# Kernel optimization log

Measured on AMD Instinct MI355X. Metric: run time of the kernel, lower is better.

Reference implementation:

```python
import jax, jax.numpy as jnp
import numpy as np


def _cofactor_antieq(M):
    """ith output = M[...,i,0] * (-1)**i * det(M with row i and col 0 deleted).

    M: (..., n, n) -> (..., n). Vectorized form of the original per-row
    jnp.delete + stack + det construction.
    """
    n = M.shape[-1]
    # rows[i] = all row indices except i, shape (n, n-1)
    rows = np.stack([np.delete(np.arange(n), i) for i in range(n)])
    Msub = M[..., 1:]                 # delete first column: (..., n, n-1)
    sub = Msub[..., rows, :]          # delete row i per output: (..., n, n-1, n-1)
    signs = jnp.asarray((-1.0) ** np.arange(n), dtype=M.dtype)
    return M[..., 0] * signs * jnp.linalg.det(sub)


def setup_inputs() -> dict:
    key = jax.random.key(0)
    ks = jax.random.split(key, 6)
    B, NSPIN, NPS, D, NION, DIM = 4096, 2, 16, 256, 8, 3
    eq_inputs = jax.random.normal(ks[0], (B, NSPIN * NPS, D), jnp.float32)
    r_ei = jax.random.normal(ks[1], (B, NSPIN * NPS, NION, DIM), jnp.float32)
    # per-spin linear orbital params (stacked over spin since splits are equal)
    W = jax.random.normal(ks[2], (NSPIN, D, NPS), jnp.float32) / np.sqrt(D)
    b = jax.random.normal(ks[3], (NSPIN, NPS), jnp.float32) * 0.01
    # anisotropic envelope decay matrices A per (spin, ion, orbital), near identity
    env_dim = jax.random.normal(ks[4], (NSPIN, NION, NPS, DIM, DIM), jnp.float32) * 0.1 + jnp.eye(DIM, dtype=jnp.float32)
    # linear combination over ions per (spin, orbital)
    env_ion = jax.random.normal(ks[5], (NSPIN, NION, NPS), jnp.float32) / NION
    return dict(eq_inputs=eq_inputs, r_ei=r_ei, W=W, b=b, env_dim=env_dim, env_ion=env_ion)


def reference(eq_inputs, r_ei, W, b, env_dim, env_ion):
    B = eq_inputs.shape[0]
    nspin, d, nps = W.shape
    nion, dim = r_ei.shape[-2], r_ei.shape[-1]
    # split particles by spin: (B, nspin, nps, ...)
    xs = eq_inputs.reshape(B, nspin, nps, d)
    rs = r_ei.reshape(B, nspin, nps, nion, dim)
    # linear part of orbitals: (B, s, n, o) with n = o = nps (square per spin)
    y = jnp.einsum('bsnd,sdo->bsno', xs, W) + b[:, None, :]
    # anisotropic exponential envelope: exp(-||A (r - R)||), summed over ions
    Ar = jnp.einsum('sioed,bsnid->bsnioe', env_dim, rs)        # (B,s,n,ion,orb,3)
    env = jnp.einsum('bsnio,sio->bsno',
                     jnp.exp(-jnp.linalg.norm(Ar, axis=-1)), env_ion)
    M = y * env                                                 # (B, s, n, n)
    cof = _cofactor_antieq(M)                                   # (B, s, n)
    return cof[..., None]                                       # (B, s, n, 1)
```

## Files before the change

### kernel.cpp

```cpp
#include <hip/hip_runtime.h>
#include <math.h>


__global__ __launch_bounds__(256)
void cof_fused(const float* __restrict__ eq,
               const float* __restrict__ rei,
               const float* __restrict__ Wm,
               const float* __restrict__ bb,
               const float* __restrict__ edim,
               const float* __restrict__ eion,
               float* __restrict__ out)
{
  __shared__ __align__(16) float Gl[8 * 6 * 16];
  __shared__ __align__(16) float Xl[4 * 2048];

  const int tid   = threadIdx.x;
  const int lane  = tid & 63;
  const int wv    = tid >> 6;
  const int blk   = blockIdx.x;
  const int sp    = blk >> 10;
  const int bbase = (blk & 1023) * 4;

  if (tid < 128) {
    const int i = tid >> 4, o = tid & 15;
    const float* A = edim + (((size_t)sp * 8 + i) * 16 + o) * 9;
    const float a0=A[0],a1=A[1],a2=A[2],a3=A[3],a4=A[4],a5=A[5],a6=A[6],a7=A[7],a8=A[8];
    float* Gp = Gl + i * 96 + o;
    Gp[0]  = a0*a0 + a3*a3 + a6*a6;
    Gp[16] = a1*a1 + a4*a4 + a7*a7;
    Gp[32] = a2*a2 + a5*a5 + a8*a8;
    Gp[48] = 2.f*(a0*a1 + a3*a4 + a6*a7);
    Gp[64] = 2.f*(a0*a2 + a3*a5 + a6*a8);
    Gp[80] = 2.f*(a1*a2 + a4*a5 + a7*a8);
  }
  __syncthreads();

  const int bidx = bbase + wv;
  const int cch  = lane >> 4;
  const int nb   = (lane >> 2) & 3;
  const int ob   = lane & 3;

  const float* xb = eq + ((size_t)bidx * 32 + sp * 16) * 256;
  const float* wb = Wm + (size_t)sp * 4096;
  float* xw = Xl + wv * 2048;

  const int srow = 2 * 0 + (lane >> 5);
  const int schk = lane & 31;

  float acc[4][4] = {{0.f,0.f,0.f,0.f},{0.f,0.f,0.f,0.f},
                     {0.f,0.f,0.f,0.f},{0.f,0.f,0.f,0.f}};

  float4 st[8];
  #pragma unroll
  for (int t = 0; t < 8; ++t)
    st[t] = *(const float4*)(xb + (2 * t + (lane >> 5)) * 256 + schk * 4);
  #pragma unroll
  for (int t = 0; t < 8; ++t) {
    const int row = 2 * t + (lane >> 5);
    *(float4*)(xw + row * 128 + (schk ^ (row & 7)) * 4) = st[t];
  }
  float4 st2[8];
  #pragma unroll
  for (int t = 0; t < 8; ++t)
    st2[t] = *(const float4*)(xb + (2 * t + (lane >> 5)) * 256 + 128 + schk * 4);

  #pragma unroll 2
  for (int q = 0; q < 8; ++q) {
    const int d0 = q * 16 + cch * 4;
    float xr[4][4], wr[4][4];
    #pragma unroll
    for (int r = 0; r < 4; ++r) {
      const int n = 4 * nb + r;
      float4 t = *(const float4*)(xw + n * 128 + ((q * 4 + cch) ^ (n & 7)) * 4);
      xr[r][0]=t.x; xr[r][1]=t.y; xr[r][2]=t.z; xr[r][3]=t.w;
    }
    #pragma unroll
    for (int j = 0; j < 4; ++j) {
      float4 t = *(const float4*)(wb + (d0 + j) * 16 + 4 * ob);
      wr[j][0]=t.x; wr[j][1]=t.y; wr[j][2]=t.z; wr[j][3]=t.w;
    }
    #pragma unroll
    for (int r = 0; r < 4; ++r)
      #pragma unroll
      for (int j = 0; j < 4; ++j)
        #pragma unroll
        for (int c2 = 0; c2 < 4; ++c2)
          acc[r][c2] = fmaf(xr[r][j], wr[j][c2], acc[r][c2]);
  }

  #pragma unroll
  for (int t = 0; t < 8; ++t) {
    const int row = 2 * t + (lane >> 5);
    *(float4*)(xw + row * 128 + (schk ^ (row & 7)) * 4) = st2[t];
  }
  #pragma unroll 2
  for (int q = 0; q < 8; ++q) {
    const int d0 = 128 + q * 16 + cch * 4;
    float xr[4][4], wr[4][4];
    #pragma unroll
    for (int r = 0; r < 4; ++r) {
      const int n = 4 * nb + r;
      float4 t = *(const float4*)(xw + n * 128 + ((q * 4 + cch) ^ (n & 7)) * 4);
      xr[r][0]=t.x; xr[r][1]=t.y; xr[r][2]=t.z; xr[r][3]=t.w;
    }
    #pragma unroll
    for (int j = 0; j < 4; ++j) {
      float4 t = *(const float4*)(wb + (d0 + j) * 16 + 4 * ob);
      wr[j][0]=t.x; wr[j][1]=t.y; wr[j][2]=t.z; wr[j][3]=t.w;
    }
    #pragma unroll
    for (int r = 0; r < 4; ++r)
      #pragma unroll
      for (int j = 0; j < 4; ++j)
        #pragma unroll
        for (int c2 = 0; c2 < 4; ++c2)
          acc[r][c2] = fmaf(xr[r][j], wr[j][c2], acc[r][c2]);
  }

  #pragma unroll
  for (int r = 0; r < 4; ++r)
    #pragma unroll
    for (int c2 = 0; c2 < 4; ++c2) {
      float v = acc[r][c2];
      v += __shfl_xor(v, 16);
      v += __shfl_xor(v, 32);
      acc[r][c2] = v;
    }

  float* Mw = xw;
  {
    float4 bv = *(const float4*)(bb + sp * 16 + 4 * ob);
    if (lane < 16) {
      #pragma unroll
      for (int r = 0; r < 4; ++r) {
        float4 v = make_float4(acc[r][0] + bv.x, acc[r][1] + bv.y,
                               acc[r][2] + bv.z, acc[r][3] + bv.w);
        *(float4*)(Mw + (4 * nb + r) * 20 + 4 * ob) = v;
      }
    }
  }

  {
    const int n = lane >> 2;
    const float* rp = rei + ((size_t)bidx * 32 + sp * 16 + n) * 24;
    float rv[24];
    #pragma unroll
    for (int t4 = 0; t4 < 6; ++t4) {
      float4 t = *(const float4*)(rp + t4 * 4);
      rv[t4*4+0]=t.x; rv[t4*4+1]=t.y; rv[t4*4+2]=t.z; rv[t4*4+3]=t.w;
    }
    float4 env = make_float4(0.f, 0.f, 0.f, 0.f);
    #pragma unroll
    for (int i = 0; i < 8; ++i) {
      const float r0 = rv[i*3], r1 = rv[i*3+1], r2 = rv[i*3+2];
      const float rr0 = r0*r0, rr1 = r1*r1, rr2 = r2*r2;
      const float rr3 = r0*r1, rr4 = r0*r2, rr5 = r1*r2;
      const float* Gp = Gl + i * 96 + 4 * ob;
      const float4 q00 = *(const float4*)(Gp);
      const float4 q11 = *(const float4*)(Gp + 16);
      const float4 q22 = *(const float4*)(Gp + 32);
      const float4 q01 = *(const float4*)(Gp + 48);
      const float4 q02 = *(const float4*)(Gp + 64);
      const float4 q12 = *(const float4*)(Gp + 80);
      const float4 io  = *(const float4*)(eion + ((size_t)sp * 8 + i) * 16 + 4 * ob);
#define ENVC(c) { float n2 = q00.c*rr0 + q11.c*rr1 + q22.c*rr2 \
                           + q01.c*rr3 + q02.c*rr4 + q12.c*rr5; \
                  n2 = fmaxf(n2, 0.f); \
                  env.c += __expf(-sqrtf(n2)) * io.c; }
      ENVC(x) ENVC(y) ENVC(z) ENVC(w)
#undef ENVC
    }
    float* mp = Mw + n * 20 + 4 * ob;
    float4 y = *(const float4*)mp;
    *(float4*)mp = make_float4(y.x * env.x, y.y * env.y, y.z * env.z, y.w * env.w);
  }
  __syncthreads();

  if (wv == 0) {
    const int g  = lane >> 4;
    const int r  = lane & 15;
    const int gb = lane & 48;
    const float* mg = Xl + g * 2048;
    float a[16];
    #pragma unroll
    for (int c = 0; c < 16; ++c) a[c] = mg[c * 20 + r];

    float det = 1.0f;
    int sign = 0;
    unsigned retired = 0;
    int piv[16];
    int srr = 0;
    float accf = (r == 0) ? 1.0f : 0.0f;
    float acc2 = 0.0f;

    #pragma unroll
    for (int k = 0; k < 16; ++k) {
      const bool act = ((retired >> r) & 1u) == 0u;
      const float av = act ? fabsf(a[k]) : 0.0f;
      unsigned pk = (__float_as_uint(av) & 0xFFFFFFF0u) | (unsigned)r;
      #pragma unroll
      for (int m = 1; m <= 8; m <<= 1) {
        unsigned o2 = __shfl_xor(pk, m);
        pk = (pk > o2) ? pk : o2;
      }
      const int p = (int)(pk & 15u);
      piv[k] = p;
      float pv = __shfl(a[k], gb | p);
      if (fabsf(pv) < 1e-30f) pv = (pv < 0.0f) ? -1e-30f : 1e-30f;
      det *= pv;
      retired |= (1u << p);
      sign ^= (int)(__popc((~retired) & ((1u << p) - 1u)) & 1u);
      if (r == p) srr = k;
      const bool upd = act && (r != p);
      float m2 = 0.0f;
      if (upd) { m2 = a[k] / pv; a[k] = m2; }
      #pragma unroll
      for (int c = k + 1; c < 16; ++c) {
        float bcv = __shfl(a[c], gb | p);
        if (upd) a[c] = fmaf(-m2, bcv, a[c]);
      }
      float zk = __shfl(accf, gb | p);
      if (r == p) acc2 = zk;
      if (upd) accf = fmaf(-m2, zk, accf);
    }
    if (sign) det = -det;

    float myx = 0.0f;
    #pragma unroll
    for (int j = 15; j >= 0; --j) {
      float t = acc2 / a[j];
      float xj = __shfl(t, gb | piv[j]);
      if (srr < j) acc2 = fmaf(-a[j], xj, acc2);
      if (r == j) myx = xj;
    }

    const float mi0 = mg[r * 20];
    const float cof = mi0 * det * myx;
    out[((size_t)(bbase + g) * 2 + sp) * 16 + r] = cof;
  }
}

extern "C" void kernel_launch(void* const* d_in, const int* in_sizes, int n_in,
                              void* d_out, int out_size, void* d_ws, size_t ws_size,
                              hipStream_t stream) {
  (void)in_sizes; (void)n_in; (void)out_size; (void)d_ws; (void)ws_size;
  const float* eq   = (const float*)d_in[0];
  const float* rei  = (const float*)d_in[1];
  const float* Wm   = (const float*)d_in[2];
  const float* bb   = (const float*)d_in[3];
  const float* edim = (const float*)d_in[4];
  const float* eion = (const float*)d_in[5];
  float* out = (float*)d_out;
  hipLaunchKernelGGL(cof_fused, dim3(2048), dim3(256), 0, stream,
                     eq, rei, Wm, bb, edim, eion, out);
}
```

Before: 231.1 us.

## Shrink LDS staging, pipeline quarter loads, and run determinant per wave

Cuts the per-wave LDS staging buffer in half by streaming the 256-wide input in four 64-column quarters with double-buffered register loads overlapping compute. Drops the block barrier and the wave-0-only determinant phase, so each wave now computes the determinant of its own matrix, with only lanes 0-15 storing results. Packs pivot indices into two registers instead of an array and requests 7 waves per EU via launch bounds. These aim at higher occupancy and less serialization, at the cost of each wave doing redundant 4x-replicated determinant work across lane groups and added register pressure from the occupancy hint.

New measurement: 300.4 us. +30.0%, slower.

```diff
diff --git a/kernel.cpp b/kernel.cpp
--- a/kernel.cpp
+++ b/kernel.cpp
@@ -2,7 +2,7 @@
 #include <math.h>
 
 
-__global__ __launch_bounds__(256)
+__global__ __launch_bounds__(256, 7)
 void cof_fused(const float* __restrict__ eq,
                const float* __restrict__ rei,
                const float* __restrict__ Wm,
@@ -12,7 +12,7 @@
                float* __restrict__ out)
 {
   __shared__ __align__(16) float Gl[8 * 6 * 16];
-  __shared__ __align__(16) float Xl[4 * 2048];
+  __shared__ __align__(16) float Xl[4 * 1024];
 
   const int tid   = threadIdx.x;
   const int lane  = tid & 63;
@@ -42,80 +42,70 @@
 
   const float* xb = eq + ((size_t)bidx * 32 + sp * 16) * 256;
   const float* wb = Wm + (size_t)sp * 4096;
-  float* xw = Xl + wv * 2048;
-
-  const int srow = 2 * 0 + (lane >> 5);
-  const int schk = lane & 31;
+  float* xw = Xl + wv * 1024;
+
+  const int srow = lane >> 4;
+  const int schk = lane & 15;
 
   float acc[4][4] = {{0.f,0.f,0.f,0.f},{0.f,0.f,0.f,0.f},
                      {0.f,0.f,0.f,0.f},{0.f,0.f,0.f,0.f}};
 
-  float4 st[8];
-  #pragma unroll
-  for (int t = 0; t < 8; ++t)
-    st[t] = *(const float4*)(xb + (2 * t + (lane >> 5)) * 256 + schk * 4);
-  #pragma unroll
-  for (int t = 0; t < 8; ++t) {
-    const int row = 2 * t + (lane >> 5);
-    *(float4*)(xw + row * 128 + (schk ^ (row & 7)) * 4) = st[t];
-  }
-  float4 st2[8];
-  #pragma unroll
-  for (int t = 0; t < 8; ++t)
-    st2[t] = *(const float4*)(xb + (2 * t + (lane >> 5)) * 256 + 128 + schk * 4);
-
-  #pragma unroll 2
-  for (int q = 0; q < 8; ++q) {
-    const int d0 = q * 16 + cch * 4;
-    float xr[4][4], wr[4][4];
-    #pragma unroll
-    for (int r = 0; r < 4; ++r) {
-      const int n = 4 * nb + r;
-      float4 t = *(const float4*)(xw + n * 128 + ((q * 4 + cch) ^ (n & 7)) * 4);
-      xr[r][0]=t.x; xr[r][1]=t.y; xr[r][2]=t.z; xr[r][3]=t.w;
-    }
-    #pragma unroll
-    for (int j = 0; j < 4; ++j) {
-      float4 t = *(const float4*)(wb + (d0 + j) * 16 + 4 * ob);
-      wr[j][0]=t.x; wr[j][1]=t.y; wr[j][2]=t.z; wr[j][3]=t.w;
-    }
-    #pragma unroll
-    for (int r = 0; r < 4; ++r)
-      #pragma unroll
-      for (int j = 0; j < 4; ++j)
-        #pragma unroll
-        for (int c2 = 0; c2 < 4; ++c2)
-          acc[r][c2] = fmaf(xr[r][j], wr[j][c2], acc[r][c2]);
-  }
-
-  #pragma unroll
-  for (int t = 0; t < 8; ++t) {
-    const int row = 2 * t + (lane >> 5);
-    *(float4*)(xw + row * 128 + (schk ^ (row & 7)) * 4) = st2[t];
-  }
-  #pragma unroll 2
-  for (int q = 0; q < 8; ++q) {
-    const int d0 = 128 + q * 16 + cch * 4;
-    float xr[4][4], wr[4][4];
-    #pragma unroll
-    for (int r = 0; r < 4; ++r) {
-      const int n = 4 * nb + r;
-      float4 t = *(const float4*)(xw + n * 128 + ((q * 4 + cch) ^ (n & 7)) * 4);
-      xr[r][0]=t.x; xr[r][1]=t.y; xr[r][2]=t.z; xr[r][3]=t.w;
-    }
-    #pragma unroll
-    for (int j = 0; j < 4; ++j) {
-      float4 t = *(const float4*)(wb + (d0 + j) * 16 + 4 * ob);
-      wr[j][0]=t.x; wr[j][1]=t.y; wr[j][2]=t.z; wr[j][3]=t.w;
-    }
-    #pragma unroll
-    for (int r = 0; r < 4; ++r)
-      #pragma unroll
-      for (int j = 0; j < 4; ++j)
-        #pragma unroll
-        for (int c2 = 0; c2 < 4; ++c2)
-          acc[r][c2] = fmaf(xr[r][j], wr[j][c2], acc[r][c2]);
-  }
+  float4 stA[4], stB[4];
+
+#define LOADQ(dst, qq)                                                        \
+  _Pragma("unroll")                                                           \
+  for (int t = 0; t < 4; ++t)                                                 \
+    dst[t] = *(const float4*)(xb + (4 * t + srow) * 256 + (qq) * 64 + schk * 4);
+
+#define WRITEQ(src)                                                           \
+  _Pragma("unroll")                                                           \
+  for (int t = 0; t < 4; ++t) {                                               \
+    const int row_ = 4 * t + srow;                                            \
+    *(float4*)(xw + row_ * 64 + ((schk ^ (row_ & 7)) * 4)) = src[t];          \
+  }
+
+#define COMPQ(qq)                                                             \
+  _Pragma("unroll")                                                           \
+  for (int g = 0; g < 4; ++g) {                                               \
+    const int dg = (qq) * 64 + g * 16 + cch * 4;                              \
+    float xr[4][4], wr4[4][4];                                                \
+    _Pragma("unroll")                                                         \
+    for (int r = 0; r < 4; ++r) {                                             \
+      const int n_ = 4 * nb + r;                                              \
+      float4 t = *(const float4*)(xw + n_ * 64 +                              \
+                                  (((g * 4 + cch) ^ (n_ & 7)) * 4));          \
+      xr[r][0]=t.x; xr[r][1]=t.y; xr[r][2]=t.z; xr[r][3]=t.w;                 \
+    }                                                                         \
+    _Pragma("unroll")                                                         \
+    for (int j = 0; j < 4; ++j) {                                             \
+      float4 t = *(const float4*)(wb + (dg + j) * 16 + 4 * ob);               \
+      wr4[j][0]=t.x; wr4[j][1]=t.y; wr4[j][2]=t.z; wr4[j][3]=t.w;             \
+    }                                                                         \
+    _Pragma("unroll")                                                         \
+    for (int r = 0; r < 4; ++r)                                               \
+      _Pragma("unroll")                                                       \
+      for (int j = 0; j < 4; ++j)                                             \
+        _Pragma("unroll")                                                     \
+        for (int c2 = 0; c2 < 4; ++c2)                                        \
+          acc[r][c2] = fmaf(xr[r][j], wr4[j][c2], acc[r][c2]);                \
+  }
+
+  LOADQ(stA, 0)
+  WRITEQ(stA)
+  LOADQ(stB, 1)
+  COMPQ(0)
+  WRITEQ(stB)
+  LOADQ(stA, 2)
+  COMPQ(1)
+  WRITEQ(stA)
+  LOADQ(stB, 3)
+  COMPQ(2)
+  WRITEQ(stB)
+  COMPQ(3)
+
+#undef LOADQ
+#undef WRITEQ
+#undef COMPQ
 
   #pragma unroll
   for (int r = 0; r < 4; ++r)
@@ -174,21 +164,18 @@
     float4 y = *(const float4*)mp;
     *(float4*)mp = make_float4(y.x * env.x, y.y * env.y, y.z * env.z, y.w * env.w);
   }
-  __syncthreads();
-
-  if (wv == 0) {
-    const int g  = lane >> 4;
+
+  {
     const int r  = lane & 15;
     const int gb = lane & 48;
-    const float* mg = Xl + g * 2048;
     float a[16];
     #pragma unroll
-    for (int c = 0; c < 16; ++c) a[c] = mg[c * 20 + r];
+    for (int c = 0; c < 16; ++c) a[c] = Mw[c * 20 + r];
 
     float det = 1.0f;
     int sign = 0;
     unsigned retired = 0;
-    int piv[16];
+    unsigned pp0 = 0, pp1 = 0;
     int srr = 0;
     float accf = (r == 0) ? 1.0f : 0.0f;
     float acc2 = 0.0f;
@@ -204,7 +191,8 @@
         pk = (pk > o2) ? pk : o2;
       }
       const int p = (int)(pk & 15u);
-      piv[k] = p;
+      if (k < 8) pp0 |= (unsigned)p << (4 * k);
+      else       pp1 |= (unsigned)p << (4 * (k - 8));
       float pv = __shfl(a[k], gb | p);
       if (fabsf(pv) < 1e-30f) pv = (pv < 0.0f) ? -1e-30f : 1e-30f;
       det *= pv;
@@ -229,14 +217,17 @@
     #pragma unroll
     for (int j = 15; j >= 0; --j) {
       float t = acc2 / a[j];
-      float xj = __shfl(t, gb | piv[j]);
+      const int pj = (int)(((j >= 8) ? (pp1 >> (4 * (j - 8)))
+                                     : (pp0 >> (4 * j))) & 15u);
+      float xj = __shfl(t, gb | pj);
       if (srr < j) acc2 = fmaf(-a[j], xj, acc2);
       if (r == j) myx = xj;
     }
 
-    const float mi0 = mg[r * 20];
+    const float mi0 = Mw[r * 20];
     const float cof = mi0 * det * myx;
-    out[((size_t)(bbase + g) * 2 + sp) * 16 + r] = cof;
+    if (lane < 16)
+      out[((size_t)bidx * 2 + sp) * 16 + r] = cof;
   }
 }
 
```
